# Kernel tuning notes

Measured on AMD Instinct MI355X. Metric: run time of the kernel, lower is better.

The kernel has to match this reference:

```python
import jax, jax.numpy as jnp
import numpy as np

NUM_CLASSES = 33  # labels 0..32; class 0 = background, 32 instances
EPS = 1e-06


def _lovasz_hinge_flat(logits, labels):
    # logits, labels: flat 1-D float arrays (labels in {0,1})
    signs = 2.0 * labels - 1.0
    errors = 1.0 - logits * signs
    order = jnp.argsort(-errors)            # descending sort
    errors_sorted = errors[order]
    gt_sorted = labels[order]
    gts = jnp.sum(gt_sorted)
    intersection = gts - jnp.cumsum(gt_sorted)
    union = gts + jnp.cumsum(1.0 - gt_sorted)
    jaccard = 1.0 - intersection / union
    grad = jnp.concatenate([jaccard[:1], jaccard[1:] - jaccard[:-1]])
    return jnp.dot(jax.nn.relu(errors_sorted), grad)


def _per_sample_loss(y_emb, y_sig, gt_patch):
    # y_emb: [2,H,W] float, y_sig: [1,H,W] float, gt_patch: [1,H,W] int
    # to_onehot(gt)[0, 1:] -> [N,H,W], N = NUM_CLASSES-1 instance channels
    gt_one_hot = jax.nn.one_hot(gt_patch[0], NUM_CLASSES, axis=0, dtype=y_emb.dtype)[1:]
    counts = jnp.sum(gt_one_hot, axis=(1, 2), keepdims=True)          # [N,1,1]
    # per-instance embedding centers: [2,N,1,1]
    centers = jnp.sum(gt_one_hot[None] * y_emb[:, None], axis=(2, 3), keepdims=True) / counts
    instance_sigmas = gt_one_hot[None] * y_sig[:, None]               # [1,N,H,W]
    sigmas = jnp.sum(instance_sigmas, axis=(2, 3), keepdims=True) / counts  # [1,N,1,1]
    var_sigmas = jnp.sum(((instance_sigmas - jax.lax.stop_gradient(sigmas)) * gt_one_hot) ** 2) / counts  # [N,1,1]
    center_dist = jnp.linalg.norm(centers - y_emb[:, None], axis=0)   # [N,H,W]
    probs = jnp.exp(-0.5 * (center_dist / sigmas) ** 2)               # [1,N,H,W]
    logits = (probs * 2.0 - 1.0).reshape(-1)
    labels = jnp.broadcast_to(gt_one_hot[None], probs.shape).reshape(-1)
    return _lovasz_hinge_flat(logits, labels) + jnp.mean(var_sigmas)


def setup_inputs() -> dict:
    key = jax.random.key(0)
    k1, k2, k3 = jax.random.split(key, 3)
    B, H, W = 4, 512, 512
    y_embeddings = jax.random.normal(k1, (B, 2, H, W), dtype=jnp.float32)
    y_sigma = jax.random.uniform(k2, (B, 1, H, W), dtype=jnp.float32)
    y_true = jax.random.randint(k3, (B, 1, H, W), 0, NUM_CLASSES, dtype=jnp.int64)
    return {"y_embeddings": y_embeddings, "y_sigma": y_sigma, "y_true": y_true}


def reference(y_embeddings, y_sigma, y_true):
    # Assumes every sample contains foreground (random labels over 512x512
    # guarantee this w.h.p.), so the torch `if torch.any(gt>0)` branch is taken
    # for all samples and the final loss is the mean over the batch.
    losses = jax.vmap(_per_sample_loss)(y_embeddings, y_sigma, y_true)
    return jnp.mean(losses)
```

## Files before the change

### kernel.cpp

```cpp
#include <hip/hip_runtime.h>

#define HW    262144
#define BNUM  4
#define NC    33
#define NI    32

#define NB     1024
#define BSCALE 64.0f
#define EG     4096
#define ESCALE 2048.0f

typedef unsigned long long ull;

#define W_CNTB 0
#define W_CNTF 4
#define W_FINL 8
#define W_HIST 16
#define W_PART (W_HIST + BNUM * 128 * NB)
#define PJ 168
#define PS (128 * PJ)

__global__ void __launch_bounds__(256) stats_kernel(
    const float* __restrict__ emb, const float* __restrict__ sig,
    const int* __restrict__ gt, float* __restrict__ ws) {
  int s = blockIdx.y;
  int j = blockIdx.x;
  int t = threadIdx.x;
  int w = t >> 6;
  __shared__ float acc[4][165];
  int bid = s * 128 + j;
  unsigned* wsu = (unsigned*)ws;
  if (bid == 0 && t < 16) wsu[t] = 0u;
  for (int k = t; k < 4 * 165; k += 256) ((float*)acc)[k] = 0.f;
  __syncthreads();
  const float* e0p = emb + (size_t)s * 2 * HW;
  const float* e1p = e0p + HW;
  const float* sp  = sig + (size_t)s * HW;
  const int*   gp  = gt  + (size_t)s * HW;
  #pragma unroll
  for (int i = 0; i < 2; ++i) {
    int idx = j * 2048 + i * 1024 + t * 4;
    int4   lb = *(const int4*)(gp + idx);
    float4 x  = *(const float4*)(e0p + idx);
    float4 y  = *(const float4*)(e1p + idx);
    float4 sg = *(const float4*)(sp + idx);
#define ACC(L, X, Y, SG)                                                   \
    if (L > 0) {                                                           \
      atomicAdd(&acc[w][L], X);        atomicAdd(&acc[w][33 + L], Y);      \
      atomicAdd(&acc[w][66 + L], SG);  atomicAdd(&acc[w][99 + L], (SG)*(SG)); \
      atomicAdd(&acc[w][132 + L], 1.0f);                                   \
    }
    ACC(lb.x, x.x, y.x, sg.x)
    ACC(lb.y, x.y, y.y, sg.y)
    ACC(lb.z, x.z, y.z, sg.z)
    ACC(lb.w, x.w, y.w, sg.w)
#undef ACC
  }
  __syncthreads();
  if (t < 165) {
    float v = acc[0][t] + acc[1][t] + acc[2][t] + acc[3][t];
    ws[W_PART + s * PS + j * PJ + t] = v;
  }
}

__global__ void __launch_bounds__(512) hist_scan_kernel(
    const float* __restrict__ emb, const int* __restrict__ gt,
    float* __restrict__ ws, float* __restrict__ out) {
  int s  = blockIdx.y;
  int lb = blockIdx.x;
  __shared__ unsigned hist[EG * 2];
  __shared__ float sums[165];
  __shared__ float4 cons[NC];
  __shared__ ull wsum[8];
  __shared__ float red[8];
  __shared__ float vart_s;
  __shared__ int flag;
  int t = threadIdx.x;
  int lane = t & 63, wid = t >> 6;
  for (int k = t; k < NB * 4; k += 512) hist[k] = 0u;
  if (t < 165) {
    const float* pp = ws + W_PART + s * PS + t;
    float sum = 0.f;
    #pragma unroll 8
    for (int j = 0; j < 128; ++j) sum += pp[j * PJ];
    sums[t] = sum;
  }
  __syncthreads();
  if (t >= 1 && t < NC) {
    float c = sums[132 + t];
    float4 C;
    if (c > 0.f) {
      float inv = 1.0f / c;
      float c0 = sums[t] * inv, c1 = sums[33 + t] * inv, sgm = sums[66 + t] * inv;
      float Q = 0.5f / (sgm * sgm) * BSCALE;
      C.x = Q; C.y = -2.0f * Q * c0; C.z = -2.0f * Q * c1;
      C.w = Q * (c0 * c0 + c1 * c1);
    } else {
      C.x = 0.f; C.y = 0.f; C.z = 0.f; C.w = (float)NB;
    }
    cons[t] = C;
  }
  __syncthreads();
  const float* e0p = emb + (size_t)s * 2 * HW;
  const float* e1p = e0p + HW;
  const int*   gp  = gt  + (size_t)s * HW;
  int idx = lb * 2048 + t * 4;
  int4   lbl = *(const int4*)(gp + idx);
  float4 px  = *(const float4*)(e0p + idx);
  float4 py  = *(const float4*)(e1p + idx);
  float4 ss;
  ss.x = fmaf(px.x, px.x, py.x * py.x);
  ss.y = fmaf(px.y, px.y, py.y * py.y);
  ss.z = fmaf(px.z, px.z, py.z * py.z);
  ss.w = fmaf(px.w, px.w, py.w * py.w);
  unsigned* hr = hist + (t & 3);
#define POSFIX(P0, P1, SV, L)                                            \
    if (L > 0) {                                                         \
      float4 C = cons[L];                                                \
      float bf = fmaf(C.x, SV, fmaf(C.y, P0, fmaf(C.z, P1, C.w)));       \
      int ib = min((int)bf, NB - 1);                                     \
      atomicAdd(&hr[ib << 2], 0xFFFFu);                                  \
    }
  POSFIX(px.x, py.x, ss.x, lbl.x)
  POSFIX(px.y, py.y, ss.y, lbl.y)
  POSFIX(px.z, py.z, ss.z, lbl.z)
  POSFIX(px.w, py.w, ss.w, lbl.w)
#undef POSFIX
  #pragma unroll 4
  for (int n = 1; n <= NI; ++n) {
    float4 C = cons[n];
#define ITEM(P0, P1, SV)                                               \
    {                                                                  \
      float bf = fmaf(C.x, SV, fmaf(C.y, P0, fmaf(C.z, P1, C.w)));     \
      int ib = min((int)bf, NB - 1);                                   \
      atomicAdd(&hr[ib << 2], 1u);                                     \
    }
    ITEM(px.x, py.x, ss.x)
    ITEM(px.y, py.y, ss.y)
    ITEM(px.z, py.z, ss.z)
    ITEM(px.w, py.w, ss.w)
#undef ITEM
  }
  __syncthreads();
  unsigned* gh = (unsigned*)ws + W_HIST + (s * 128 + lb) * NB;
  for (int k = t; k < NB; k += 512) {
    unsigned v = hist[k * 4] + hist[k * 4 + 1] + hist[k * 4 + 2] + hist[k * 4 + 3];
    __hip_atomic_store(&gh[k], v, __ATOMIC_RELAXED, __HIP_MEMORY_SCOPE_AGENT);
  }
  __syncthreads();
  if (t == 0) {
    __threadfence();
    flag = (__hip_atomic_fetch_add((unsigned*)ws + W_CNTB + s, 1u,
              __ATOMIC_ACQ_REL, __HIP_MEMORY_SCOPE_AGENT) == 127u);
  }
  __syncthreads();
  if (!flag) return;

  unsigned* ep = hist;
  unsigned* en = hist + EG;
  for (int k = t; k < 2 * EG; k += 512) hist[k] = 0u;
  if (wid == 0) {
    float S = 0.f, rcp = 0.f;
    if (lane >= 1 && lane < NC) {
      float c = sums[132 + lane];
      if (c > 0.f) {
        float sg = sums[66 + lane] / c;
        S = sums[99 + lane] - c * sg * sg;
        rcp = 1.0f / c;
      }
    }
    for (int o = 32; o; o >>= 1) {
      S   += __shfl_down(S, o);
      rcp += __shfl_down(rcp, o);
    }
    if (lane == 0) vart_s = S * rcp / (float)NI;
  }
  __syncthreads();
  unsigned* ghs = (unsigned*)ws + W_HIST + s * 128 * NB;
  for (int b = t; b < NB; b += 512) {
    unsigned pos = 0, neg = 0;
    #pragma unroll 16
    for (int j = 0; j < 128; ++j) {
      unsigned v = __hip_atomic_load(&ghs[j * NB + b],
                     __ATOMIC_RELAXED, __HIP_MEMORY_SCOPE_AGENT);
      pos += v >> 16;
      neg += v & 0xFFFFu;
    }
    if (pos | neg) {
      float tc = ((float)b + 0.5f) * (1.0f / BSCALE);
      float ex = __expf(-tc);
      if (pos) {
        float e = 2.0f - 2.0f * ex;
        int k = (int)(e * ESCALE); if (k > EG - 1) k = EG - 1;
        atomicAdd(&ep[k], pos);
      }
      if (neg) {
        float e = 2.0f * ex;
        int k = (int)(e * ESCALE); if (k > EG - 1) k = EG - 1;
        atomicAdd(&en[k], neg);
      }
    }
  }
  __syncthreads();
  const int CH = EG / 512;
  int j0 = t * CH;
  unsigned np = 0, nn = 0;
  for (int k = 0; k < CH; ++k) {
    int b = EG - 1 - (j0 + k);
    np += ep[b]; nn += en[b];
  }
  ull v = ((ull)np << 32) | (ull)nn;
  ull inc = v;
  for (int o = 1; o < 64; o <<= 1) {
    ull u = __shfl_up(inc, o);
    if (lane >= o) inc += u;
  }
  if (lane == 63) wsum[wid] = inc;
  __syncthreads();
  ull offset = 0, total = 0;
  for (int i = 0; i < 8; ++i) {
    ull xr = wsum[i];
    if (i < wid) offset += xr;
    total += xr;
  }
  ull excl = offset + inc - v;
  float P = (float)(unsigned)(total >> 32);
  unsigned p = (unsigned)(excl >> 32), f = (unsigned)(excl & 0xFFFFFFFFu);
  float jprev = 1.0f - (P - (float)p) / (P + (float)f);
  float contrib = 0.f;
  for (int k = 0; k < CH; ++k) {
    int b = EG - 1 - (j0 + k);
    unsigned ap_ = ep[b], an_ = en[b];
    if (ap_ | an_) {
      p += ap_; f += an_;
      float j = 1.0f - (P - (float)p) / (P + (float)f);
      float e = ((float)b + 0.5f) * (2.0f / EG);
      contrib += e * (j - jprev);
      jprev = j;
    }
  }
  for (int o = 32; o; o >>= 1) contrib += __shfl_down(contrib, o);
  if (lane == 0) red[wid] = contrib;
  __syncthreads();
  if (t == 0) {
    float tot = 0.f;
    for (int i = 0; i < 8; ++i) tot += red[i];
    float loss = tot + vart_s;
    float* fin = ws + W_FINL;
    atomicExch(&fin[s], loss);
    __threadfence();
    unsigned old = atomicAdd((unsigned*)ws + W_CNTF, 1u);
    if (old == BNUM - 1) {
      float a = 0.f;
      for (int i = 0; i < BNUM; ++i) a += atomicAdd(&fin[i], 0.0f);
      out[0] = a * (1.0f / BNUM);
    }
  }
}

extern "C" void kernel_launch(void* const* d_in, const int* in_sizes, int n_in,
                              void* d_out, int out_size, void* d_ws, size_t ws_size,
                              hipStream_t stream) {
  const float* emb = (const float*)d_in[0];
  const float* sig = (const float*)d_in[1];
  const int*   gt  = (const int*)d_in[2];
  float* out = (float*)d_out;
  float* ws  = (float*)d_ws;

  dim3 gA(128, BNUM);
  stats_kernel<<<gA, 256, 0, stream>>>(emb, sig, gt, ws);
  dim3 gB(128, BNUM);
  hist_scan_kernel<<<gB, 512, 0, stream>>>(emb, gt, ws, out);
}
```

Measured before the change: 133.2 us.

## Split histogram merge into parallel third kernel instead of last-block serial merge

The histogram kernel previously had the last-arriving block per sample serially merge 128 partial histograms of 1024 bins, which is a long single-block tail. That merge now runs in a separate kernel where each wavefront reduces one bin across the 128 partials (stored transposed) and scatters into a global energy grid with atomics. Only the final scan stays in one block per sample. The change also widens the shared-memory histogram replication from 4 to 8 copies to cut atomic contention, and splits the partial-stats reduction over two thread groups. It adds a kernel launch, global atomics and an extra workspace region.

Result: faster. 129.7 us (-2.6%).

```diff
diff --git a/kernel.cpp b/kernel.cpp
--- a/kernel.cpp
+++ b/kernel.cpp
@@ -12,11 +12,13 @@
 
 typedef unsigned long long ull;
 
-#define W_CNTB 0
+#define W_CNTC 0
 #define W_CNTF 4
 #define W_FINL 8
-#define W_HIST 16
-#define W_PART (W_HIST + BNUM * 128 * NB)
+#define W_VART 12
+#define W_EGRID 16
+#define W_HIST  (W_EGRID + BNUM * 2 * EG)
+#define W_PART  (W_HIST + BNUM * 128 * NB)
 #define PJ 168
 #define PS (128 * PJ)
 
@@ -30,6 +32,7 @@
   __shared__ float acc[4][165];
   int bid = s * 128 + j;
   unsigned* wsu = (unsigned*)ws;
+  if (t < 64) wsu[W_EGRID + bid * 64 + t] = 0u;
   if (bid == 0 && t < 16) wsu[t] = 0u;
   for (int k = t; k < 4 * 165; k += 256) ((float*)acc)[k] = 0.f;
   __syncthreads();
@@ -63,28 +66,29 @@
   }
 }
 
-__global__ void __launch_bounds__(512) hist_scan_kernel(
+__global__ void __launch_bounds__(512) hist_kernel(
     const float* __restrict__ emb, const int* __restrict__ gt,
-    float* __restrict__ ws, float* __restrict__ out) {
+    float* __restrict__ ws) {
   int s  = blockIdx.y;
   int lb = blockIdx.x;
-  __shared__ unsigned hist[EG * 2];
+  int t = threadIdx.x;
+  int lane = t & 63, wid = t >> 6;
+  __shared__ unsigned hist[NB * 8];
+  __shared__ float sums2[2][165];
   __shared__ float sums[165];
   __shared__ float4 cons[NC];
-  __shared__ ull wsum[8];
-  __shared__ float red[8];
-  __shared__ float vart_s;
-  __shared__ int flag;
-  int t = threadIdx.x;
-  int lane = t & 63, wid = t >> 6;
-  for (int k = t; k < NB * 4; k += 512) hist[k] = 0u;
-  if (t < 165) {
-    const float* pp = ws + W_PART + s * PS + t;
+  for (int k = t; k < NB * 8; k += 512) hist[k] = 0u;
+  if (t < 330) {
+    int r = (t >= 165) ? 1 : 0;
+    int c = t - r * 165;
+    const float* pp = ws + W_PART + s * PS + (r << 6) * PJ + c;
     float sum = 0.f;
-    #pragma unroll 8
-    for (int j = 0; j < 128; ++j) sum += pp[j * PJ];
-    sums[t] = sum;
-  }
+    #pragma unroll 16
+    for (int jj = 0; jj < 64; ++jj) sum += pp[jj * PJ];
+    sums2[r][c] = sum;
+  }
+  __syncthreads();
+  if (t < 165) sums[t] = sums2[0][t] + sums2[1][t];
   __syncthreads();
   if (t >= 1 && t < NC) {
     float c = sums[132 + t];
@@ -99,6 +103,22 @@
       C.x = 0.f; C.y = 0.f; C.z = 0.f; C.w = (float)NB;
     }
     cons[t] = C;
+  }
+  if (lb == 0 && wid == 0) {
+    float S = 0.f, rcp = 0.f;
+    if (lane >= 1 && lane < NC) {
+      float c = sums[132 + lane];
+      if (c > 0.f) {
+        float sg = sums[66 + lane] / c;
+        S = sums[99 + lane] - c * sg * sg;
+        rcp = 1.0f / c;
+      }
+    }
+    for (int o = 32; o; o >>= 1) {
+      S   += __shfl_down(S, o);
+      rcp += __shfl_down(rcp, o);
+    }
+    if (lane == 0) ws[W_VART + s] = S * rcp / (float)NI;
   }
   __syncthreads();
   const float* e0p = emb + (size_t)s * 2 * HW;
@@ -113,13 +133,13 @@
   ss.y = fmaf(px.y, px.y, py.y * py.y);
   ss.z = fmaf(px.z, px.z, py.z * py.z);
   ss.w = fmaf(px.w, px.w, py.w * py.w);
-  unsigned* hr = hist + (t & 3);
+  unsigned* hr = hist + (t & 7);
 #define POSFIX(P0, P1, SV, L)                                            \
     if (L > 0) {                                                         \
       float4 C = cons[L];                                                \
       float bf = fmaf(C.x, SV, fmaf(C.y, P0, fmaf(C.z, P1, C.w)));       \
       int ib = min((int)bf, NB - 1);                                     \
-      atomicAdd(&hr[ib << 2], 0xFFFFu);                                  \
+      atomicAdd(&hr[ib << 3], 0xFFFFu);                                  \
     }
   POSFIX(px.x, py.x, ss.x, lbl.x)
   POSFIX(px.y, py.y, ss.y, lbl.y)
@@ -133,7 +153,7 @@
     {                                                                  \
       float bf = fmaf(C.x, SV, fmaf(C.y, P0, fmaf(C.z, P1, C.w)));     \
       int ib = min((int)bf, NB - 1);                                   \
-      atomicAdd(&hr[ib << 2], 1u);                                     \
+      atomicAdd(&hr[ib << 3], 1u);                                     \
     }
     ITEM(px.x, py.x, ss.x)
     ITEM(px.y, py.y, ss.y)
@@ -142,72 +162,69 @@
 #undef ITEM
   }
   __syncthreads();
-  unsigned* gh = (unsigned*)ws + W_HIST + (s * 128 + lb) * NB;
+  unsigned* gh = (unsigned*)ws + W_HIST + s * (128 * NB);
   for (int k = t; k < NB; k += 512) {
-    unsigned v = hist[k * 4] + hist[k * 4 + 1] + hist[k * 4 + 2] + hist[k * 4 + 3];
-    __hip_atomic_store(&gh[k], v, __ATOMIC_RELAXED, __HIP_MEMORY_SCOPE_AGENT);
+    uint4 a = *(uint4*)&hist[k * 8];
+    uint4 b = *(uint4*)&hist[k * 8 + 4];
+    gh[k * 128 + lb] = a.x + a.y + a.z + a.w + b.x + b.y + b.z + b.w;
+  }
+}
+
+__global__ void __launch_bounds__(512) merge_scan_kernel(
+    float* __restrict__ ws, float* __restrict__ out) {
+  int s  = blockIdx.y;
+  int lb = blockIdx.x;
+  int t = threadIdx.x;
+  int lane = t & 63, wid = t >> 6;
+  __shared__ unsigned eg[EG * 2];
+  __shared__ ull wsum[8];
+  __shared__ float red[8];
+  __shared__ int flag;
+  unsigned* gh = (unsigned*)ws + W_HIST + s * (128 * NB);
+  int b = lb * 8 + wid;
+  unsigned v0 = gh[b * 128 + lane];
+  unsigned v1 = gh[b * 128 + 64 + lane];
+  ull pv = ((ull)((v0 >> 16) + (v1 >> 16)) << 32)
+         | (ull)((v0 & 0xFFFFu) + (v1 & 0xFFFFu));
+  for (int o = 32; o; o >>= 1) pv += __shfl_down(pv, o);
+  if (lane == 0) {
+    unsigned pos = (unsigned)(pv >> 32), neg = (unsigned)(pv & 0xFFFFFFFFu);
+    unsigned* egp = (unsigned*)ws + W_EGRID + s * 2 * EG;
+    unsigned* egn = egp + EG;
+    float tc = ((float)b + 0.5f) * (1.0f / BSCALE);
+    float ex = __expf(-tc);
+    if (pos) {
+      float e = 2.0f - 2.0f * ex;
+      int k = (int)(e * ESCALE); if (k > EG - 1) k = EG - 1;
+      atomicAdd(&egp[k], pos);
+    }
+    if (neg) {
+      float e = 2.0f * ex;
+      int k = (int)(e * ESCALE); if (k > EG - 1) k = EG - 1;
+      atomicAdd(&egn[k], neg);
+    }
   }
   __syncthreads();
   if (t == 0) {
     __threadfence();
-    flag = (__hip_atomic_fetch_add((unsigned*)ws + W_CNTB + s, 1u,
-              __ATOMIC_ACQ_REL, __HIP_MEMORY_SCOPE_AGENT) == 127u);
+    flag = (atomicAdd((unsigned*)ws + W_CNTC + s, 1u) == 127u);
   }
   __syncthreads();
   if (!flag) return;
 
-  unsigned* ep = hist;
-  unsigned* en = hist + EG;
-  for (int k = t; k < 2 * EG; k += 512) hist[k] = 0u;
-  if (wid == 0) {
-    float S = 0.f, rcp = 0.f;
-    if (lane >= 1 && lane < NC) {
-      float c = sums[132 + lane];
-      if (c > 0.f) {
-        float sg = sums[66 + lane] / c;
-        S = sums[99 + lane] - c * sg * sg;
-        rcp = 1.0f / c;
-      }
-    }
-    for (int o = 32; o; o >>= 1) {
-      S   += __shfl_down(S, o);
-      rcp += __shfl_down(rcp, o);
-    }
-    if (lane == 0) vart_s = S * rcp / (float)NI;
-  }
-  __syncthreads();
-  unsigned* ghs = (unsigned*)ws + W_HIST + s * 128 * NB;
-  for (int b = t; b < NB; b += 512) {
-    unsigned pos = 0, neg = 0;
-    #pragma unroll 16
-    for (int j = 0; j < 128; ++j) {
-      unsigned v = __hip_atomic_load(&ghs[j * NB + b],
-                     __ATOMIC_RELAXED, __HIP_MEMORY_SCOPE_AGENT);
-      pos += v >> 16;
-      neg += v & 0xFFFFu;
-    }
-    if (pos | neg) {
-      float tc = ((float)b + 0.5f) * (1.0f / BSCALE);
-      float ex = __expf(-tc);
-      if (pos) {
-        float e = 2.0f - 2.0f * ex;
-        int k = (int)(e * ESCALE); if (k > EG - 1) k = EG - 1;
-        atomicAdd(&ep[k], pos);
-      }
-      if (neg) {
-        float e = 2.0f * ex;
-        int k = (int)(e * ESCALE); if (k > EG - 1) k = EG - 1;
-        atomicAdd(&en[k], neg);
-      }
-    }
-  }
-  __syncthreads();
+  __threadfence();
+  unsigned* egg = (unsigned*)ws + W_EGRID + s * 2 * EG;
+  for (int k = t; k < 2 * EG; k += 512) eg[k] = egg[k];
+  float vart = ws[W_VART + s];
+  __syncthreads();
+  unsigned* ep = eg;
+  unsigned* en = eg + EG;
   const int CH = EG / 512;
   int j0 = t * CH;
   unsigned np = 0, nn = 0;
   for (int k = 0; k < CH; ++k) {
-    int b = EG - 1 - (j0 + k);
-    np += ep[b]; nn += en[b];
+    int bb = EG - 1 - (j0 + k);
+    np += ep[bb]; nn += en[bb];
   }
   ull v = ((ull)np << 32) | (ull)nn;
   ull inc = v;
@@ -229,12 +246,12 @@
   float jprev = 1.0f - (P - (float)p) / (P + (float)f);
   float contrib = 0.f;
   for (int k = 0; k < CH; ++k) {
-    int b = EG - 1 - (j0 + k);
-    unsigned ap_ = ep[b], an_ = en[b];
+    int bb = EG - 1 - (j0 + k);
+    unsigned ap_ = ep[bb], an_ = en[bb];
     if (ap_ | an_) {
       p += ap_; f += an_;
       float j = 1.0f - (P - (float)p) / (P + (float)f);
-      float e = ((float)b + 0.5f) * (2.0f / EG);
+      float e = ((float)bb + 0.5f) * (2.0f / EG);
       contrib += e * (j - jprev);
       jprev = j;
     }
@@ -245,7 +262,7 @@
   if (t == 0) {
     float tot = 0.f;
     for (int i = 0; i < 8; ++i) tot += red[i];
-    float loss = tot + vart_s;
+    float loss = tot + vart;
     float* fin = ws + W_FINL;
     atomicExch(&fin[s], loss);
     __threadfence();
@@ -267,8 +284,8 @@
   float* out = (float*)d_out;
   float* ws  = (float*)d_ws;
 
-  dim3 gA(128, BNUM);
-  stats_kernel<<<gA, 256, 0, stream>>>(emb, sig, gt, ws);
-  dim3 gB(128, BNUM);
-  hist_scan_kernel<<<gB, 512, 0, stream>>>(emb, gt, ws, out);
-}
+  dim3 g(128, BNUM);
+  stats_kernel<<<g, 256, 0, stream>>>(emb, sig, gt, ws);
+  hist_kernel<<<g, 512, 0, stream>>>(emb, gt, ws);
+  merge_scan_kernel<<<g, 512, 0, stream>>>(ws, out);
+}
```
